# Kernel tuning notes

Hardware: AMD Instinct MI355X
Metric: run time of the kernel (lower is better)

## Reference

```python
import jax, jax.numpy as jnp
import numpy as np

K = 9          # census/SAD window (block_size arg of photometric_loss)
R = K // 2
EPS = 0.5      # loss_eps


def _grid_sample_disp(pattern, disp):
    """Disparity warp: pattern_proj[b,0,v,u] = bilinear(pattern, x=u-disp, y=v).
    Matches F.grid_sample(padding_mode='border', align_corners=True) since
    uv1 = 2*(x/(W-1)-0.5) maps back to pixel coord x exactly, and y is the row index.
    pattern: [1,1,H,W], disp: [B,H,W] -> [B,1,H,W]."""
    H, W = pattern.shape[-2:]
    B = disp.shape[0]
    u0 = jnp.arange(W, dtype=disp.dtype)
    x = u0[None, None, :] - disp                 # source x coordinate, [B,H,W]
    x = jnp.clip(x, 0.0, W - 1.0)                # border padding
    x0 = jnp.floor(x)
    w = x - x0                                   # bilinear weight
    i0 = x0.astype(jnp.int32)
    i1 = jnp.minimum(i0 + 1, W - 1)
    p = jnp.broadcast_to(pattern[0, 0], (B, H, W))
    g0 = jnp.take_along_axis(p, i0, axis=2)
    g1 = jnp.take_along_axis(p, i1, axis=2)
    return ((1.0 - w) * g0 + w * g1)[:, None]    # [B,1,H,W]


def _census_sad(a, b, eps):
    """Per-pixel census-SAD over a KxK window.
    Soft census: c(n, center) = (n-center)/(eps+|n-center|); per pixel the loss is
    mean over window offsets of |c_a - c_b|, out-of-bounds offsets skipped.
    a, b: [B,1,H,W] -> [B,1,H,W]."""
    B, C, H, W = a.shape
    pa = jnp.pad(a, ((0, 0), (0, 0), (R, R), (R, R)))
    pb = jnp.pad(b, ((0, 0), (0, 0), (R, R), (R, R)))
    vm = jnp.pad(jnp.ones((H, W), a.dtype), ((R, R), (R, R)))  # validity mask
    acc = jnp.zeros_like(a)
    for dh in range(-R, R + 1):
        for dw in range(-R, R + 1):
            na = pa[:, :, R + dh:R + dh + H, R + dw:R + dw + W]
            nb = pb[:, :, R + dh:R + dh + H, R + dw:R + dw + W]
            da = na - a
            db = nb - b
            ca = da / (eps + jnp.abs(da))
            cb = db / (eps + jnp.abs(db))
            v = vm[R + dh:R + dh + H, R + dw:R + dw + W]
            acc = acc + v * jnp.abs(ca - cb)
    return acc / (K * K)


def reference(disp0, im, pattern):
    B = disp0.shape[0]
    H, W = im.shape[-2:]
    d = disp0.reshape(B, H, W)
    pattern_proj = _grid_sample_disp(pattern, d)
    diff = _census_sad(pattern_proj, im, EPS)
    mask = jnp.ones_like(im)                     # std is None
    val = (mask * diff).sum() / mask.sum()
    return val, pattern_proj


def setup_inputs():
    key = jax.random.key(0)
    k1, k2, k3 = jax.random.split(key, 3)
    B, H, W = 32, 512, 640
    disp0 = jax.random.uniform(k1, (B, 1, H, W), dtype=jnp.float32) * 64.0
    im = jax.random.uniform(k2, (B, 1, H, W), dtype=jnp.float32)
    pattern = jax.random.uniform(k3, (1, 1, H, W), dtype=jnp.float32)
    return {"disp0": disp0, "im": im, "pattern": pattern}
```

## Files before the change

kernel.cpp:

```cpp
#include <hip/hip_runtime.h>

#define Wd 640
#define Hd 512
#define NB 32
#define TW 64
#define TH 16
#define RR 4
#define SW 76
constexpr int TILES_X = Wd / TW;
constexpr int TILES_Y = Hd / TH;
constexpr float EPSC = 0.5f;

__global__ __launch_bounds__(256)
void warp_kernel(const float* __restrict__ disp, const float* __restrict__ pattern,
                 float* __restrict__ proj)
{
    int gid = blockIdx.x * 256 + threadIdx.x;
    int n = gid * 4;
    float4 d4 = *(const float4*)(disp + n);
    int u = n % Wd;
    int rowbase = ((n / Wd) % Hd) * Wd;
    float dv[4] = {d4.x, d4.y, d4.z, d4.w};
    #pragma unroll
    for (int j = 0; j < 4; ++j) {
        float x = (float)(u + j) - dv[j];
        x = fminf(fmaxf(x, 0.f), (float)(Wd - 1));
        float x0 = floorf(x);
        float w = x - x0;
        int i0 = (int)x0;
        int i1 = min(i0 + 1, Wd - 1);
        float g0 = pattern[rowbase + i0];
        float g1 = pattern[rowbase + i1];
        proj[n + j] = fmaf(w, g1 - g0, g0);
    }
}

__device__ __forceinline__ void census_ne(float na, float nb, float ac, float bc,
                                          float& n, float& e)
{
    float da = na - ac;
    float db = nb - bc;
    float d1 = EPSC + fabsf(da);
    float d2 = EPSC + fabsf(db);
    n = fmaf(da, d2, -(db * d1));
    e = d1 * d2;
}

__device__ __forceinline__ float comb4(float n1, float e1, float n2, float e2,
                                       float n3, float e3, float n4, float e4)
{
    float e12 = e1 * e2, e34 = e3 * e4;
    float s12 = fmaf(fabsf(n2), e1, fabsf(n1) * e2);
    float s34 = fmaf(fabsf(n4), e3, fabsf(n3) * e4);
    float t   = fmaf(s34, e12, s12 * e34);
    return t * __builtin_amdgcn_rcpf(e12 * e34);
}

#define GRP4(ACC, xA0,xA1,xA2,xA3, xB0,xB1,xB2,xB3) { \
    float n0,e0,n1,e1,n2,e2,n3,e3;                    \
    census_ne(xA0,xB0,ca0,cb0,n0,e0);                 \
    census_ne(xA1,xB1,ca1,cb1,n1,e1);                 \
    census_ne(xA2,xB2,ca2,cb2,n2,e2);                 \
    census_ne(xA3,xB3,ca3,cb3,n3,e3);                 \
    ACC += comb4(n0,e0,n1,e1,n2,e2,n3,e3); }

#define GRPM(ACC, DW, xA0,xA1,xA2,xA3, xB0,xB1,xB2,xB3) { \
    float n0,e0,n1,e1,n2,e2,n3,e3;                    \
    census_ne(xA0,xB0,ca0,cb0,n0,e0);                 \
    census_ne(xA1,xB1,ca1,cb1,n1,e1);                 \
    census_ne(xA2,xB2,ca2,cb2,n2,e2);                 \
    census_ne(xA3,xB3,ca3,cb3,n3,e3);                 \
    n0 *= ((unsigned)(ub+0+(DW)) < (unsigned)Wd) ? mv : 0.f; \
    n1 *= ((unsigned)(ub+1+(DW)) < (unsigned)Wd) ? mv : 0.f; \
    n2 *= ((unsigned)(ub+2+(DW)) < (unsigned)Wd) ? mv : 0.f; \
    n3 *= ((unsigned)(ub+3+(DW)) < (unsigned)Wd) ? mv : 0.f; \
    ACC += comb4(n0,e0,n1,e1,n2,e2,n3,e3); }

#define LOADROW(row)                                              \
    float4 tA0 = *(const float4*)&sa[row][4 * tx];                \
    float4 tA1 = *(const float4*)&sa[row][4 * tx + 4];            \
    float4 tA2 = *(const float4*)&sa[row][4 * tx + 8];            \
    float4 tB0 = *(const float4*)&sb[row][4 * tx];                \
    float4 tB1 = *(const float4*)&sb[row][4 * tx + 4];            \
    float4 tB2 = *(const float4*)&sb[row][4 * tx + 8];            \
    float ra0=tA0.x, ra1=tA0.y, ra2 =tA0.z, ra3 =tA0.w;           \
    float ra4=tA1.x, ra5=tA1.y, ra6 =tA1.z, ra7 =tA1.w;           \
    float ra8=tA2.x, ra9=tA2.y, ra10=tA2.z, ra11=tA2.w;           \
    float rb0=tB0.x, rb1=tB0.y, rb2 =tB0.z, rb3 =tB0.w;           \
    float rb4=tB1.x, rb5=tB1.y, rb6 =tB1.z, rb7 =tB1.w;           \
    float rb8=tB2.x, rb9=tB2.y, rb10=tB2.z, rb11=tB2.w;

#define NINE_GRPS(GM)                                             \
    GM(acc0, -4, ra0,ra1,ra2 ,ra3 , rb0,rb1,rb2 ,rb3 )            \
    GM(acc1, -3, ra1,ra2,ra3 ,ra4 , rb1,rb2,rb3 ,rb4 )            \
    GM(acc0, -2, ra2,ra3,ra4 ,ra5 , rb2,rb3,rb4 ,rb5 )            \
    GM(acc1, -1, ra3,ra4,ra5 ,ra6 , rb3,rb4,rb5 ,rb6 )            \
    GM(acc0,  0, ra4,ra5,ra6 ,ra7 , rb4,rb5,rb6 ,rb7 )            \
    GM(acc1,  1, ra5,ra6,ra7 ,ra8 , rb5,rb6,rb7 ,rb8 )            \
    GM(acc0,  2, ra6,ra7,ra8 ,ra9 , rb6,rb7,rb8 ,rb9 )            \
    GM(acc1,  3, ra7,ra8,ra9 ,ra10, rb7,rb8,rb9 ,rb10)            \
    GM(acc0,  4, ra8,ra9,ra10,ra11, rb8,rb9,rb10,rb11)

#define GRP4_NODW(ACC, DW, xA0,xA1,xA2,xA3, xB0,xB1,xB2,xB3) \
    GRP4(ACC, xA0,xA1,xA2,xA3, xB0,xB1,xB2,xB3)

__global__ __launch_bounds__(256)
void census_kernel(const float* __restrict__ proj, const float* __restrict__ im,
                   float* __restrict__ partial)
{
    __shared__ float sa[TH + RR][SW];
    __shared__ float sb[TH + RR][SW];

    const int tU = blockIdx.x, tV = blockIdx.y, b = blockIdx.z;
    const int tid = threadIdx.x;
    const float* pb = proj + (size_t)b * (Hd * Wd);
    const float* ib = im   + (size_t)b * (Hd * Wd);
    const int v0  = tV * TH;
    const int u0g = tU * TW - RR;

    const bool edge = (tU == 0) | (tU == TILES_X - 1) | (tV == TILES_Y - 1);

    if (!edge) {
        const float* pbase = pb + v0 * Wd + u0g;
        const float* ibase = ib + v0 * Wd + u0g;
        for (int f = tid; f < (TH + RR) * (TW + 2 * RR) / 4; f += 256) {
            int r = f / 18;
            int c = (f - 18 * r) * 4;
            *(float4*)&sa[r][c] = *(const float4*)(pbase + r * Wd + c);
            *(float4*)&sb[r][c] = *(const float4*)(ibase + r * Wd + c);
        }
    } else {
        for (int idx = tid; idx < (TH + RR) * (TW + 2 * RR); idx += 256) {
            int r = idx / (TW + 2 * RR);
            int c = idx - r * (TW + 2 * RR);
            int gv = min(v0 + r, Hd - 1);
            int gu = min(max(u0g + c, 0), Wd - 1);
            int off = gv * Wd + gu;
            sa[r][c] = pb[off];
            sb[r][c] = ib[off];
        }
    }
    __syncthreads();

    const int ty = tid >> 4;
    const int tx = tid & 15;

    float acc0 = 0.f, acc1 = 0.f;
    const int ub = tU * TW + 4 * tx;
    const int v  = v0 + ty;
    float ca0, ca1, ca2, ca3, cb0, cb1, cb2, cb3;

    if (!edge) {
        {
            LOADROW(ty)
            ca0 = ra4; ca1 = ra5; ca2 = ra6; ca3 = ra7;
            cb0 = rb4; cb1 = rb5; cb2 = rb6; cb3 = rb7;
            GRP4(acc0, ra5,ra6,ra7,ra8 , rb5,rb6,rb7,rb8 )
            GRP4(acc1, ra6,ra7,ra8,ra9 , rb6,rb7,rb8,rb9 )
            GRP4(acc0, ra7,ra8,ra9,ra10, rb7,rb8,rb9,rb10)
            GRP4(acc1, ra8,ra9,ra10,ra11, rb8,rb9,rb10,rb11)
        }
        for (int dh = 1; dh <= RR; ++dh) {
            LOADROW(ty + dh)
            NINE_GRPS(GRP4_NODW)
        }
    } else {
        {
            LOADROW(ty)
            ca0 = ra4; ca1 = ra5; ca2 = ra6; ca3 = ra7;
            cb0 = rb4; cb1 = rb5; cb2 = rb6; cb3 = rb7;
            float mv = 1.f;
            GRPM(acc0, 1, ra5,ra6,ra7,ra8 , rb5,rb6,rb7,rb8 )
            GRPM(acc1, 2, ra6,ra7,ra8,ra9 , rb6,rb7,rb8,rb9 )
            GRPM(acc0, 3, ra7,ra8,ra9,ra10, rb7,rb8,rb9,rb10)
            GRPM(acc1, 4, ra8,ra9,ra10,ra11, rb8,rb9,rb10,rb11)
        }
        for (int dh = 1; dh <= RR; ++dh) {
            LOADROW(ty + dh)
            float mv = (v + dh < Hd) ? 1.f : 0.f;
            NINE_GRPS(GRPM)
        }
    }

    float acc = acc0 + acc1;
    #pragma unroll
    for (int o = 32; o; o >>= 1) acc += __shfl_down(acc, o);
    __shared__ float wsum[4];
    int wid = tid >> 6, lane = tid & 63;
    if (lane == 0) wsum[wid] = acc;
    __syncthreads();
    if (tid == 0) {
        float s = wsum[0] + wsum[1] + wsum[2] + wsum[3];
        partial[((int)blockIdx.z * gridDim.y + blockIdx.y) * gridDim.x + blockIdx.x] = s;
    }
}

__global__ __launch_bounds__(1024)
void final_reduce(const float* __restrict__ partial, float* __restrict__ out)
{
    const int n = NB * TILES_Y * TILES_X;
    double s = 0.0;
    for (int i = threadIdx.x; i < n; i += 1024) s += (double)partial[i];
    __shared__ double sm[1024];
    sm[threadIdx.x] = s;
    __syncthreads();
    for (int st = 512; st; st >>= 1) {
        if (threadIdx.x < st) sm[threadIdx.x] += sm[threadIdx.x + st];
        __syncthreads();
    }
    if (threadIdx.x == 0) {
        out[0] = (float)(sm[0] * (2.0 / (81.0 * (double)NB * Hd * Wd)));
    }
}

extern "C" void kernel_launch(void* const* d_in, const int* in_sizes, int n_in,
                              void* d_out, int out_size, void* d_ws, size_t ws_size,
                              hipStream_t stream)
{
    const float* disp    = (const float*)d_in[0];
    const float* im      = (const float*)d_in[1];
    const float* pattern = (const float*)d_in[2];
    float* out  = (float*)d_out;
    float* proj = out + 1;
    float* partial = (float*)d_ws;

    const int npx = NB * Hd * Wd;
    warp_kernel<<<npx / (256 * 4), 256, 0, stream>>>(disp, pattern, proj);

    dim3 grid(TILES_X, TILES_Y, NB);
    census_kernel<<<grid, 256, 0, stream>>>(proj, im, partial);

    final_reduce<<<1, 1024, 0, stream>>>(partial, out);
}
```

Measured before the change: 142.9 us.

## Pack projected pattern and image as fp16 pairs for census kernel

The warp kernel now also reads the image and writes an interleaved packed-half2 copy of projected pattern and image into the workspace, alongside the fp32 projection output. The census kernel stages a single packed shared-memory tile and unpacks it to fp32 per row, halving shared-memory footprint and loads. This trades an extra global write in the warp pass for a halved read in the census pass, and adds fp16 rounding of inputs that could affect accuracy. A fallback to the old fp32 path is kept when the workspace is too small.

```diff
diff --git a/kernel.cpp b/kernel.cpp
--- a/kernel.cpp
+++ b/kernel.cpp
@@ -6,10 +6,58 @@
 #define TW 64
 #define TH 16
 #define RR 4
-#define SW 76
+#define SW 72
 constexpr int TILES_X = Wd / TW;
 constexpr int TILES_Y = Hd / TH;
+constexpr int NBLK = TILES_X * TILES_Y * NB;
+constexpr size_t HWsz = (size_t)Hd * Wd;
 constexpr float EPSC = 0.5f;
+
+typedef __fp16 h2_t __attribute__((ext_vector_type(2)));
+
+__device__ __forceinline__ unsigned pack2(float a, float b)
+{
+    union { h2_t h; unsigned u; } c;
+    c.h = __builtin_amdgcn_cvt_pkrtz(a, b);
+    return c.u;
+}
+__device__ __forceinline__ void unp2(unsigned u, float& a, float& b)
+{
+    union { unsigned u; h2_t h; } c; c.u = u;
+    a = (float)c.h[0]; b = (float)c.h[1];
+}
+
+__global__ __launch_bounds__(256)
+void warp_pack(const float* __restrict__ disp, const float* __restrict__ pattern,
+               const float* __restrict__ im, float* __restrict__ proj,
+               unsigned* __restrict__ pk)
+{
+    int gid = blockIdx.x * 256 + threadIdx.x;
+    int n = gid * 4;
+    float4 d4 = *(const float4*)(disp + n);
+    float4 i4 = *(const float4*)(im + n);
+    int u = n % Wd;
+    int rowbase = ((n / Wd) % Hd) * Wd;
+    float dv[4] = {d4.x, d4.y, d4.z, d4.w};
+    float iv[4] = {i4.x, i4.y, i4.z, i4.w};
+    float pv[4];
+    #pragma unroll
+    for (int j = 0; j < 4; ++j) {
+        float x = (float)(u + j) - dv[j];
+        x = fminf(fmaxf(x, 0.f), (float)(Wd - 1));
+        float x0 = floorf(x);
+        float w = x - x0;
+        int i0 = (int)x0;
+        int i1 = min(i0 + 1, Wd - 1);
+        float g0 = pattern[rowbase + i0];
+        float g1 = pattern[rowbase + i1];
+        pv[j] = fmaf(w, g1 - g0, g0);
+    }
+    *(float4*)(proj + n) = make_float4(pv[0], pv[1], pv[2], pv[3]);
+    uint4 o = { pack2(pv[0], iv[0]), pack2(pv[1], iv[1]),
+                pack2(pv[2], iv[2]), pack2(pv[3], iv[3]) };
+    *(uint4*)(pk + n) = o;
+}
 
 __global__ __launch_bounds__(256)
 void warp_kernel(const float* __restrict__ disp, const float* __restrict__ pattern,
@@ -76,7 +124,129 @@
     n3 *= ((unsigned)(ub+3+(DW)) < (unsigned)Wd) ? mv : 0.f; \
     ACC += comb4(n0,e0,n1,e1,n2,e2,n3,e3); }
 
-#define LOADROW(row)                                              \
+#define NINE_GRPS(GM)                                             \
+    GM(acc0, -4, ra0,ra1,ra2 ,ra3 , rb0,rb1,rb2 ,rb3 )            \
+    GM(acc1, -3, ra1,ra2,ra3 ,ra4 , rb1,rb2,rb3 ,rb4 )            \
+    GM(acc0, -2, ra2,ra3,ra4 ,ra5 , rb2,rb3,rb4 ,rb5 )            \
+    GM(acc1, -1, ra3,ra4,ra5 ,ra6 , rb3,rb4,rb5 ,rb6 )            \
+    GM(acc0,  0, ra4,ra5,ra6 ,ra7 , rb4,rb5,rb6 ,rb7 )            \
+    GM(acc1,  1, ra5,ra6,ra7 ,ra8 , rb5,rb6,rb7 ,rb8 )            \
+    GM(acc0,  2, ra6,ra7,ra8 ,ra9 , rb6,rb7,rb8 ,rb9 )            \
+    GM(acc1,  3, ra7,ra8,ra9 ,ra10, rb7,rb8,rb9 ,rb10)            \
+    GM(acc0,  4, ra8,ra9,ra10,ra11, rb8,rb9,rb10,rb11)
+
+#define GRP4_NODW(ACC, DW, xA0,xA1,xA2,xA3, xB0,xB1,xB2,xB3) \
+    GRP4(ACC, xA0,xA1,xA2,xA3, xB0,xB1,xB2,xB3)
+
+#define LOADROW_H2(row)                                           \
+    uint4 q0 = *(const uint4*)&sp[row][4 * tx];                   \
+    uint4 q1 = *(const uint4*)&sp[row][4 * tx + 4];               \
+    uint4 q2 = *(const uint4*)&sp[row][4 * tx + 8];               \
+    float ra0,ra1,ra2,ra3,ra4,ra5,ra6,ra7,ra8,ra9,ra10,ra11;      \
+    float rb0,rb1,rb2,rb3,rb4,rb5,rb6,rb7,rb8,rb9,rb10,rb11;      \
+    unp2(q0.x, ra0, rb0); unp2(q0.y, ra1, rb1);                   \
+    unp2(q0.z, ra2, rb2); unp2(q0.w, ra3, rb3);                   \
+    unp2(q1.x, ra4, rb4); unp2(q1.y, ra5, rb5);                   \
+    unp2(q1.z, ra6, rb6); unp2(q1.w, ra7, rb7);                   \
+    unp2(q2.x, ra8, rb8); unp2(q2.y, ra9, rb9);                   \
+    unp2(q2.z, ra10, rb10); unp2(q2.w, ra11, rb11);
+
+#define LOADCTR_H2(row)                                           \
+    uint4 q1 = *(const uint4*)&sp[row][4 * tx + 4];               \
+    uint4 q2 = *(const uint4*)&sp[row][4 * tx + 8];               \
+    float ra4,ra5,ra6,ra7,ra8,ra9,ra10,ra11;                      \
+    float rb4,rb5,rb6,rb7,rb8,rb9,rb10,rb11;                      \
+    unp2(q1.x, ra4, rb4); unp2(q1.y, ra5, rb5);                   \
+    unp2(q1.z, ra6, rb6); unp2(q1.w, ra7, rb7);                   \
+    unp2(q2.x, ra8, rb8); unp2(q2.y, ra9, rb9);                   \
+    unp2(q2.z, ra10, rb10); unp2(q2.w, ra11, rb11);
+
+__global__ __launch_bounds__(256)
+void census_h2(const unsigned* __restrict__ pk, float* __restrict__ partial)
+{
+    __shared__ unsigned sp[TH + RR][SW];
+
+    const int tU = blockIdx.x, tV = blockIdx.y, b = blockIdx.z;
+    const int tid = threadIdx.x;
+    const unsigned* pkb = pk + (size_t)b * HWsz;
+    const int v0  = tV * TH;
+    const int u0g = tU * TW - RR;
+
+    const bool edge = (tU == 0) | (tU == TILES_X - 1) | (tV == TILES_Y - 1);
+
+    if (!edge) {
+        const unsigned* base = pkb + v0 * Wd + u0g;
+        for (int f = tid; f < (TH + RR) * 18; f += 256) {
+            int r = f / 18;
+            int c = (f - 18 * r) * 4;
+            *(uint4*)&sp[r][c] = *(const uint4*)(base + r * Wd + c);
+        }
+    } else {
+        unsigned* spf = &sp[0][0];
+        for (int idx = tid; idx < (TH + RR) * SW; idx += 256) {
+            int r = idx / SW;
+            int c = idx - r * SW;
+            int gv = min(v0 + r, Hd - 1);
+            int gu = min(max(u0g + c, 0), Wd - 1);
+            spf[idx] = pkb[gv * Wd + gu];
+        }
+    }
+    __syncthreads();
+
+    const int ty = tid >> 4;
+    const int tx = tid & 15;
+
+    float acc0 = 0.f, acc1 = 0.f;
+    const int ub = tU * TW + 4 * tx;
+    const int v  = v0 + ty;
+    float ca0, ca1, ca2, ca3, cb0, cb1, cb2, cb3;
+
+    if (!edge) {
+        {
+            LOADCTR_H2(ty)
+            ca0 = ra4; ca1 = ra5; ca2 = ra6; ca3 = ra7;
+            cb0 = rb4; cb1 = rb5; cb2 = rb6; cb3 = rb7;
+            GRP4(acc0, ra5,ra6,ra7,ra8 , rb5,rb6,rb7,rb8 )
+            GRP4(acc1, ra6,ra7,ra8,ra9 , rb6,rb7,rb8,rb9 )
+            GRP4(acc0, ra7,ra8,ra9,ra10, rb7,rb8,rb9,rb10)
+            GRP4(acc1, ra8,ra9,ra10,ra11, rb8,rb9,rb10,rb11)
+        }
+        for (int dh = 1; dh <= RR; ++dh) {
+            LOADROW_H2(ty + dh)
+            NINE_GRPS(GRP4_NODW)
+        }
+    } else {
+        {
+            LOADCTR_H2(ty)
+            ca0 = ra4; ca1 = ra5; ca2 = ra6; ca3 = ra7;
+            cb0 = rb4; cb1 = rb5; cb2 = rb6; cb3 = rb7;
+            float mv = 1.f;
+            GRPM(acc0, 1, ra5,ra6,ra7,ra8 , rb5,rb6,rb7,rb8 )
+            GRPM(acc1, 2, ra6,ra7,ra8,ra9 , rb6,rb7,rb8,rb9 )
+            GRPM(acc0, 3, ra7,ra8,ra9,ra10, rb7,rb8,rb9,rb10)
+            GRPM(acc1, 4, ra8,ra9,ra10,ra11, rb8,rb9,rb10,rb11)
+        }
+        for (int dh = 1; dh <= RR; ++dh) {
+            LOADROW_H2(ty + dh)
+            float mv = (v + dh < Hd) ? 1.f : 0.f;
+            NINE_GRPS(GRPM)
+        }
+    }
+
+    float acc = acc0 + acc1;
+    #pragma unroll
+    for (int o = 32; o; o >>= 1) acc += __shfl_down(acc, o);
+    __shared__ float wsum[4];
+    int wid = tid >> 6, lane = tid & 63;
+    if (lane == 0) wsum[wid] = acc;
+    __syncthreads();
+    if (tid == 0) {
+        float s = wsum[0] + wsum[1] + wsum[2] + wsum[3];
+        partial[((int)blockIdx.z * gridDim.y + blockIdx.y) * gridDim.x + blockIdx.x] = s;
+    }
+}
+
+#define LOADROW_F(row)                                            \
     float4 tA0 = *(const float4*)&sa[row][4 * tx];                \
     float4 tA1 = *(const float4*)&sa[row][4 * tx + 4];            \
     float4 tA2 = *(const float4*)&sa[row][4 * tx + 8];            \
@@ -90,31 +260,17 @@
     float rb4=tB1.x, rb5=tB1.y, rb6 =tB1.z, rb7 =tB1.w;           \
     float rb8=tB2.x, rb9=tB2.y, rb10=tB2.z, rb11=tB2.w;
 
-#define NINE_GRPS(GM)                                             \
-    GM(acc0, -4, ra0,ra1,ra2 ,ra3 , rb0,rb1,rb2 ,rb3 )            \
-    GM(acc1, -3, ra1,ra2,ra3 ,ra4 , rb1,rb2,rb3 ,rb4 )            \
-    GM(acc0, -2, ra2,ra3,ra4 ,ra5 , rb2,rb3,rb4 ,rb5 )            \
-    GM(acc1, -1, ra3,ra4,ra5 ,ra6 , rb3,rb4,rb5 ,rb6 )            \
-    GM(acc0,  0, ra4,ra5,ra6 ,ra7 , rb4,rb5,rb6 ,rb7 )            \
-    GM(acc1,  1, ra5,ra6,ra7 ,ra8 , rb5,rb6,rb7 ,rb8 )            \
-    GM(acc0,  2, ra6,ra7,ra8 ,ra9 , rb6,rb7,rb8 ,rb9 )            \
-    GM(acc1,  3, ra7,ra8,ra9 ,ra10, rb7,rb8,rb9 ,rb10)            \
-    GM(acc0,  4, ra8,ra9,ra10,ra11, rb8,rb9,rb10,rb11)
-
-#define GRP4_NODW(ACC, DW, xA0,xA1,xA2,xA3, xB0,xB1,xB2,xB3) \
-    GRP4(ACC, xA0,xA1,xA2,xA3, xB0,xB1,xB2,xB3)
-
 __global__ __launch_bounds__(256)
-void census_kernel(const float* __restrict__ proj, const float* __restrict__ im,
-                   float* __restrict__ partial)
+void census_f32(const float* __restrict__ proj, const float* __restrict__ im,
+                float* __restrict__ partial)
 {
     __shared__ float sa[TH + RR][SW];
     __shared__ float sb[TH + RR][SW];
 
     const int tU = blockIdx.x, tV = blockIdx.y, b = blockIdx.z;
     const int tid = threadIdx.x;
-    const float* pb = proj + (size_t)b * (Hd * Wd);
-    const float* ib = im   + (size_t)b * (Hd * Wd);
+    const float* pb = proj + (size_t)b * HWsz;
+    const float* ib = im   + (size_t)b * HWsz;
     const int v0  = tV * TH;
     const int u0g = tU * TW - RR;
 
@@ -123,16 +279,16 @@
     if (!edge) {
         const float* pbase = pb + v0 * Wd + u0g;
         const float* ibase = ib + v0 * Wd + u0g;
-        for (int f = tid; f < (TH + RR) * (TW + 2 * RR) / 4; f += 256) {
+        for (int f = tid; f < (TH + RR) * 18; f += 256) {
             int r = f / 18;
             int c = (f - 18 * r) * 4;
             *(float4*)&sa[r][c] = *(const float4*)(pbase + r * Wd + c);
             *(float4*)&sb[r][c] = *(const float4*)(ibase + r * Wd + c);
         }
     } else {
-        for (int idx = tid; idx < (TH + RR) * (TW + 2 * RR); idx += 256) {
-            int r = idx / (TW + 2 * RR);
-            int c = idx - r * (TW + 2 * RR);
+        for (int idx = tid; idx < (TH + RR) * SW; idx += 256) {
+            int r = idx / SW;
+            int c = idx - r * SW;
             int gv = min(v0 + r, Hd - 1);
             int gu = min(max(u0g + c, 0), Wd - 1);
             int off = gv * Wd + gu;
@@ -152,7 +308,7 @@
 
     if (!edge) {
         {
-            LOADROW(ty)
+            LOADROW_F(ty)
             ca0 = ra4; ca1 = ra5; ca2 = ra6; ca3 = ra7;
             cb0 = rb4; cb1 = rb5; cb2 = rb6; cb3 = rb7;
             GRP4(acc0, ra5,ra6,ra7,ra8 , rb5,rb6,rb7,rb8 )
@@ -161,12 +317,12 @@
             GRP4(acc1, ra8,ra9,ra10,ra11, rb8,rb9,rb10,rb11)
         }
         for (int dh = 1; dh <= RR; ++dh) {
-            LOADROW(ty + dh)
+            LOADROW_F(ty + dh)
             NINE_GRPS(GRP4_NODW)
         }
     } else {
         {
-            LOADROW(ty)
+            LOADROW_F(ty)
             ca0 = ra4; ca1 = ra5; ca2 = ra6; ca3 = ra7;
             cb0 = rb4; cb1 = rb5; cb2 = rb6; cb3 = rb7;
             float mv = 1.f;
@@ -176,7 +332,7 @@
             GRPM(acc1, 4, ra8,ra9,ra10,ra11, rb8,rb9,rb10,rb11)
         }
         for (int dh = 1; dh <= RR; ++dh) {
-            LOADROW(ty + dh)
+            LOADROW_F(ty + dh)
             float mv = (v + dh < Hd) ? 1.f : 0.f;
             NINE_GRPS(GRPM)
         }
@@ -198,9 +354,8 @@
 __global__ __launch_bounds__(1024)
 void final_reduce(const float* __restrict__ partial, float* __restrict__ out)
 {
-    const int n = NB * TILES_Y * TILES_X;
     double s = 0.0;
-    for (int i = threadIdx.x; i < n; i += 1024) s += (double)partial[i];
+    for (int i = threadIdx.x; i < NBLK; i += 1024) s += (double)partial[i];
     __shared__ double sm[1024];
     sm[threadIdx.x] = s;
     __syncthreads();
@@ -222,13 +377,20 @@
     const float* pattern = (const float*)d_in[2];
     float* out  = (float*)d_out;
     float* proj = out + 1;
-    float* partial = (float*)d_ws;
-
-    const int npx = NB * Hd * Wd;
-    warp_kernel<<<npx / (256 * 4), 256, 0, stream>>>(disp, pattern, proj);
-
+    const int npx = NB * (int)HWsz;
     dim3 grid(TILES_X, TILES_Y, NB);
-    census_kernel<<<grid, 256, 0, stream>>>(proj, im, partial);
-
-    final_reduce<<<1, 1024, 0, stream>>>(partial, out);
-}
+
+    const size_t need = HWsz * NB * sizeof(unsigned) + NBLK * sizeof(float);
+    if (ws_size >= need) {
+        unsigned* pk   = (unsigned*)d_ws;
+        float* partial = (float*)(pk + HWsz * NB);
+        warp_pack<<<npx / (256 * 4), 256, 0, stream>>>(disp, pattern, im, proj, pk);
+        census_h2<<<grid, 256, 0, stream>>>(pk, partial);
+        final_reduce<<<1, 1024, 0, stream>>>(partial, out);
+    } else {
+        float* partial = (float*)d_ws;
+        warp_kernel<<<npx / (256 * 4), 256, 0, stream>>>(disp, pattern, proj);
+        census_f32<<<grid, 256, 0, stream>>>(proj, im, partial);
+        final_reduce<<<1, 1024, 0, stream>>>(partial, out);
+    }
+}
```

After: 156.2 us. 1.09x slower.
